# Performance work log

Measured on AMD Instinct MI355X. Metric: run time of the kernel, lower is better.

Reference implementation:

```python
import jax, jax.numpy as jnp
import numpy as np

B, C, H, W = 2, 128, 64, 64


def setup_inputs() -> dict:
    key = jax.random.key(0)
    ks = jax.random.split(key, 16)
    s = 1.0 / np.sqrt(C)
    d = {
        "x": jax.random.normal(ks[0], (B, C, H, W), jnp.float32),
        "y": jax.random.normal(ks[1], (B, C, H, W), jnp.float32),
    }
    names = ["qr", "qi", "kr", "ki", "vr", "vi"]
    for i, n in enumerate(names):
        d["W" + n] = jax.random.normal(ks[2 + 2 * i], (C, C), jnp.float32) * s
        d["b" + n] = jax.random.normal(ks[3 + 2 * i], (C,), jnp.float32) * s
    return d


def _lin(t, Wt, bt):
    # t: [b, n, c]; torch Linear: t @ W^T + b
    return jnp.einsum("bnc,dc->bnd", t, Wt) + bt


def reference(x, y, Wqr, bqr, Wqi, bqi, Wkr, bkr, Wki, bki, Wvr, bvr, Wvi, bvi):
    b, c, h, w = x.shape
    xf = jnp.fft.fft2(x)  # over last two axes (h, w)
    yf = jnp.fft.fft2(y)
    # b c h w -> b (h w) c
    def flat(t):
        return t.transpose(0, 2, 3, 1).reshape(b, h * w, c)
    xr, xi = flat(xf.real), flat(xf.imag)
    yr, yi = flat(yf.real), flat(yf.imag)

    Qr = _lin(xr, Wqr, bqr) - _lin(xi, Wqi, bqi)
    Qi = _lin(xi, Wqr, bqr) + _lin(xr, Wqi, bqi)
    Kr = _lin(yr, Wkr, bkr) - _lin(yi, Wki, bki)
    Ki = _lin(yi, Wkr, bkr) + _lin(yr, Wki, bki)
    Vr = _lin(yr, Wvr, bvr) - _lin(yi, Wvi, bvi)
    Vi = _lin(yi, Wvr, bvr) + _lin(yr, Wvi, bvi)

    sr = jnp.einsum("bnc,bmc->bnm", Qr, Kr) - jnp.einsum("bnc,bmc->bnm", Qi, Ki)
    si = jnp.einsum("bnc,bmc->bnm", Qr, Ki) + jnp.einsum("bnc,bmc->bnm", Qi, Kr)
    scores = jnp.sqrt(sr * sr + si * si + 1e-8)
    attn = jax.nn.softmax(scores, axis=-1)

    out_r = jnp.einsum("bnm,bmc->bnc", attn, Vr)
    out_i = jnp.einsum("bnm,bmc->bnc", attn, Vi)
    out_c = jax.lax.complex(out_r, out_i)
    # b (h w) c -> b c h w
    out_c = out_c.reshape(b, h, w, c).transpose(0, 3, 1, 2)
    return jnp.fft.ifft2(out_c).real
```

## Files before the change

kernel.cpp:

```cpp
#include <hip/hip_runtime.h>
#include <math.h>


#define PI2 6.283185307179586f

typedef __attribute__((ext_vector_type(8))) short short8;
typedef __attribute__((ext_vector_type(4))) float f32x4;

#define MFMA16(A,B,C) __builtin_amdgcn_mfma_f32_16x16x32_bf16((A),(B),(C),0,0,0)

__device__ inline unsigned short f2bf(float x){
  union{float f; unsigned int u;} a; a.f = x;
  unsigned int r = (a.u + 0x7fffu + ((a.u>>16)&1u)) >> 16;
  return (unsigned short)r;
}
__device__ inline float bf2f(unsigned short h){
  union{unsigned int u; float f;} a; a.u = ((unsigned int)h)<<16; return a.f;
}
__device__ inline short8 neg8(short8 x){
  union{short8 v; unsigned int u[4];} a; a.v = x;
  a.u[0]^=0x80008000u; a.u[1]^=0x80008000u; a.u[2]^=0x80008000u; a.u[3]^=0x80008000u;
  return a.v;
}
__device__ inline void gload_lds16(const void* g, void* lds){
  __builtin_amdgcn_global_load_lds((const __attribute__((address_space(1))) unsigned int*)g,
                                   (__attribute__((address_space(3))) unsigned int*)lds,
                                   16, 0, 0);
}

__global__ __launch_bounds__(256) void dft2_fwd_kernel(
    const float* __restrict__ x, const float* __restrict__ y,
    float* __restrict__ xr, float* __restrict__ xi,
    float* __restrict__ yr, float* __restrict__ yi)
{
  __shared__ float Xs[4096];
  __shared__ float Tr[4096], Ti[4096];
  __shared__ float twc[64], tws[64];
  int blk = blockIdx.x;
  const float* src; float *outr, *outi;
  int plane;
  if (blk < 256) { src = x; outr = xr; outi = xi; plane = blk; }
  else           { src = y; outr = yr; outi = yi; plane = blk - 256; }
  int b = plane >> 7, c = plane & 127;
  int t = threadIdx.x;
  if (t < 64) {
    float ang = -PI2 * (float)t / 64.0f;
    twc[t] = cosf(ang); tws[t] = sinf(ang);
  }
  const float* p = src + ((size_t)plane << 12);
  for (int i = t; i < 4096; i += 256) Xs[i] = p[i];
  __syncthreads();
  for (int j = 0; j < 16; j++) {
    int o = t + 256 * j; int h = o >> 6, wp = o & 63;
    float ar = 0.f, ai = 0.f;
    for (int w = 0; w < 64; w++) {
      int k = (w * wp) & 63;
      float v = Xs[h * 64 + w];
      ar = fmaf(v, twc[k], ar);
      ai = fmaf(v, tws[k], ai);
    }
    Tr[h * 64 + wp] = ar; Ti[h * 64 + wp] = ai;
  }
  __syncthreads();
  size_t ob = ((size_t)b * 4096) * 128 + c;
  for (int j = 0; j < 16; j++) {
    int o = t + 256 * j; int hp = o >> 6, wp = o & 63;
    float ar = 0.f, ai = 0.f;
    for (int h = 0; h < 64; h++) {
      int k = (h * hp) & 63;
      float cr = twc[k], ci = tws[k];
      float tr = Tr[h * 64 + wp], ti = Ti[h * 64 + wp];
      ar += tr * cr - ti * ci;
      ai += tr * ci + ti * cr;
    }
    int n = (hp << 6) + wp;
    outr[ob + (size_t)n * 128] = ar;
    outi[ob + (size_t)n * 128] = ai;
  }
}

__global__ __launch_bounds__(256) void proj_kernel(
    const float* __restrict__ xr, const float* __restrict__ xi,
    const float* __restrict__ yr, const float* __restrict__ yi,
    const float* __restrict__ Wqr, const float* __restrict__ bqr,
    const float* __restrict__ Wqi, const float* __restrict__ bqi,
    const float* __restrict__ Wkr, const float* __restrict__ bkr,
    const float* __restrict__ Wki, const float* __restrict__ bki,
    const float* __restrict__ Wvr, const float* __restrict__ bvr,
    const float* __restrict__ Wvi, const float* __restrict__ bvi,
    unsigned short* __restrict__ FQ, unsigned short* __restrict__ FK,
    unsigned short* __restrict__ FV)
{
  __shared__ float Asr[64 * 33], Asi[64 * 33], Wsr[128 * 33], Wsi[128 * 33];
  int nt = blockIdx.x, lin = blockIdx.y, b = blockIdx.z;
  const float *ar, *ai, *Wr, *Wi, *br_, *bi_;
  unsigned short* F;
  if (lin == 0)      { ar = xr; ai = xi; Wr = Wqr; Wi = Wqi; br_ = bqr; bi_ = bqi; F = FQ; }
  else if (lin == 1) { ar = yr; ai = yi; Wr = Wkr; Wi = Wki; br_ = bkr; bi_ = bki; F = FK; }
  else               { ar = yr; ai = yi; Wr = Wvr; Wi = Wvi; br_ = bvr; bi_ = bvi; F = FV; }
  int t = threadIdx.x; int td = t & 15, tn = t >> 4;
  int n0 = nt * 64;
  size_t abase = (size_t)b * 4096 * 128 + (size_t)n0 * 128;
  const size_t PS = (size_t)2 * 4096 * 128;
  float accr[4][8] = {}, acci[4][8] = {};
  for (int kk = 0; kk < 4; kk++) {
    __syncthreads();
    for (int idx = t; idx < 64 * 32; idx += 256) {
      int r = idx >> 5, ccol = idx & 31;
      Asr[r * 33 + ccol] = ar[abase + (size_t)r * 128 + kk * 32 + ccol];
      Asi[r * 33 + ccol] = ai[abase + (size_t)r * 128 + kk * 32 + ccol];
    }
    for (int idx = t; idx < 128 * 32; idx += 256) {
      int r = idx >> 5, ccol = idx & 31;
      Wsr[r * 33 + ccol] = Wr[(size_t)r * 128 + kk * 32 + ccol];
      Wsi[r * 33 + ccol] = Wi[(size_t)r * 128 + kk * 32 + ccol];
    }
    __syncthreads();
    for (int k = 0; k < 32; k++) {
      float a_r[4], a_i[4], w_r[8], w_i[8];
      #pragma unroll
      for (int i = 0; i < 4; i++) {
        a_r[i] = Asr[(tn * 4 + i) * 33 + k];
        a_i[i] = Asi[(tn * 4 + i) * 33 + k];
      }
      #pragma unroll
      for (int jj = 0; jj < 8; jj++) {
        w_r[jj] = Wsr[(td + 16 * jj) * 33 + k];
        w_i[jj] = Wsi[(td + 16 * jj) * 33 + k];
      }
      #pragma unroll
      for (int i = 0; i < 4; i++)
        #pragma unroll
        for (int jj = 0; jj < 8; jj++) {
          accr[i][jj] += a_r[i] * w_r[jj] - a_i[i] * w_i[jj];
          acci[i][jj] += a_i[i] * w_r[jj] + a_r[i] * w_i[jj];
        }
    }
  }
  for (int jj = 0; jj < 8; jj++) {
    int d = td + 16 * jj;
    float brd = br_[d], bid = bi_[d];
    #pragma unroll
    for (int i = 0; i < 4; i++) {
      int n = n0 + tn * 4 + i;
      float cr = accr[i][jj] + (brd - bid);
      float ci = acci[i][jj] + (brd + bid);
      size_t base = ((size_t)b * 4096 + n) * 128 + d;
      if (lin <= 1) {
        unsigned short rh = f2bf(cr); unsigned short rl = f2bf(cr - bf2f(rh));
        unsigned short ih = f2bf(ci); unsigned short il = f2bf(ci - bf2f(ih));
        F[0 * PS + base] = rh;
        F[1 * PS + base] = rl;
        F[2 * PS + base] = ih;
        F[3 * PS + base] = il;
      } else {
        F[0 * PS + base] = f2bf(cr);
        F[1 * PS + base] = f2bf(ci);
      }
    }
  }
}

__global__ __launch_bounds__(256) void kpack_kernel(
    const unsigned short* __restrict__ F, unsigned short* __restrict__ Kpk)
{
  int blk = blockIdx.x;
  int b = blk >> 6, mt = blk & 63;
  int t = threadIdx.x;
  size_t obase = (size_t)blk * 4096;
  #pragma unroll
  for (int k = 0; k < 16; k++) {
    int idx = t + 256 * k;
    int l = idx & 63, s = (idx >> 6) & 3, tml = (idx >> 8) & 3, a = idx >> 10;
    int n = mt * 64 + tml * 16 + (l & 15);
    int c0 = 32 * s + 8 * (l >> 4);
    const short8 v = *(const short8*)(F + (((size_t)(a * 2 + b) * 4096 + n) * 128 + c0));
    *(short8*)(Kpk + (obase + idx) * 8) = v;
  }
}

__global__ __launch_bounds__(256) void vpack32_kernel(
    const unsigned short* __restrict__ F, unsigned short* __restrict__ Vpk)
{
  __shared__ unsigned short Vs[2][128][128];
  int blk = blockIdx.x;
  int b = blk >> 5, mtp = blk & 31;
  int t = threadIdx.x;
  const size_t PS = (size_t)2 * 4096 * 128;
  #pragma unroll
  for (int k = 0; k < 16; k++) {
    int idx = t + 256 * k;
    int c8 = idx & 15, row = (idx >> 4) & 127, p = idx >> 11;
    short8 v = *(const short8*)(F + (size_t)p * PS +
                ((size_t)(b * 4096) + mtp * 128 + row) * 128 + c8 * 8);
    *(short8*)(&Vs[p][row][c8 * 8]) = v;
  }
  __syncthreads();
  size_t obase = (size_t)blk * 4096;
  #pragma unroll
  for (int k = 0; k < 16; k++) {
    int idx = t + 256 * k;
    int l2 = idx & 63, tc = (idx >> 6) & 15, w2 = idx >> 10;
    int g2 = l2 >> 4, c2 = l2 & 15;
    int cc = tc * 16 + c2; int p = cc >> 7; int cv = cc & 127;
    int rbase = (g2 >> 1) * 64 + 16 * w2 + 8 * (g2 & 1);
    short8 v;
    #pragma unroll
    for (int j = 0; j < 8; j++) v[j] = (short)Vs[p][rbase + j][cv];
    *(short8*)(Vpk + (obase + idx) * 8) = v;
  }
}

__global__ __launch_bounds__(256, 2) void attn_mfma_kernel(
    const unsigned short* __restrict__ FQ, const unsigned short* __restrict__ Kpk,
    const unsigned short* __restrict__ Vpk,
    float* __restrict__ Or_, float* __restrict__ Oi_)
{
  __shared__ __align__(16) short Klds[4][8192];
  __shared__ __align__(16) unsigned short Ppriv[4][16 * 40];
  __shared__ float Msh[4][16];
  __shared__ float Lsh[4][16];

  const int bi = blockIdx.x;
  const int xg = bi & 7;
  const int b = xg >> 2;
  const int qt2 = (bi >> 3) * 4 + (xg & 3);
  const int t = threadIdx.x;
  const int w = t >> 6, l = t & 63;
  const int g = l >> 4, c = l & 15;

  const size_t PS = (size_t)2 * 4096 * 128;
  short8 Qf[4][4];
  #pragma unroll
  for (int a = 0; a < 4; a++)
    #pragma unroll
    for (int s = 0; s < 4; s++)
      Qf[a][s] = *(const short8*)(FQ + (size_t)a * PS +
                 ((size_t)(b * 4096) + qt2 * 16 + c) * 128 + 32 * s + 8 * g);

  f32x4 O[16], Oe;
  #pragma unroll
  for (int tc = 0; tc < 16; tc++) O[tc] = (f32x4){0.f, 0.f, 0.f, 0.f};
  Oe = (f32x4){0.f, 0.f, 0.f, 0.f};
  float Mq = -3e38f;
  const short b1 = (short)0x3F80;
  const short8 ones = {b1, b1, b1, b1, b1, b1, b1, b1};
  const short8* Vp8 = (const short8*)Vpk;

  const char* KpkB = (const char*)Kpk;
  char* chunkB = (char*)&Klds[w][0];
  const short8* chunk8 = (const short8*)&Klds[w][0];

  auto STAGE = [&](int tile) {
    const char* src = KpkB + ((size_t)(b * 64 + tile) << 16);
    #pragma unroll
    for (int a = 0; a < 4; a++)
      #pragma unroll
      for (int s = 0; s < 4; s++)
        gload_lds16(src + (((a * 4 + w) * 4 + s) << 10) + l * 16,
                    chunkB + ((a * 4 + s) << 10));
  };

  STAGE(0);
  asm volatile("s_waitcnt vmcnt(0)" ::: "memory");
  __builtin_amdgcn_sched_barrier(0);

  f32x4 sE, sO;
  for (int mt = 0; mt < 64; mt++) {
    f32x4 sr = (f32x4){0, 0, 0, 0}, si = (f32x4){0, 0, 0, 0};
    #pragma unroll
    for (int s = 0; s < 4; s++) {
      short8 Arh = chunk8[(0 * 4 + s) * 64 + l];
      short8 Arl = chunk8[(1 * 4 + s) * 64 + l];
      short8 Aih = chunk8[(2 * 4 + s) * 64 + l];
      short8 Ail = chunk8[(3 * 4 + s) * 64 + l];
      short8 nqh = neg8(Qf[2][s]);
      short8 nql = neg8(Qf[3][s]);
      sr = MFMA16(Arh, Qf[0][s], sr);
      si = MFMA16(Arh, Qf[2][s], si);
      sr = MFMA16(Arh, Qf[1][s], sr);
      si = MFMA16(Arh, Qf[3][s], si);
      sr = MFMA16(Arl, Qf[0][s], sr);
      si = MFMA16(Arl, Qf[2][s], si);
      sr = MFMA16(Aih, nqh, sr);
      si = MFMA16(Aih, Qf[0][s], si);
      sr = MFMA16(Aih, nql, sr);
      si = MFMA16(Aih, Qf[1][s], si);
      sr = MFMA16(Ail, nqh, sr);
      si = MFMA16(Ail, Qf[0][s], si);
    }
    f32x4 s0;
    #pragma unroll
    for (int r = 0; r < 4; r++)
      s0[r] = sqrtf(sr[r] * sr[r] + si[r] * si[r] + 1e-8f);
    asm volatile("s_waitcnt lgkmcnt(0)" ::: "memory");
    __builtin_amdgcn_sched_barrier(0);
    if (mt + 1 < 64) STAGE(mt + 1);
    if ((mt & 1) == 0) {
      sE = s0;
    } else {
      sO = s0;
      float mloc = fmaxf(fmaxf(fmaxf(sE[0], sE[1]), fmaxf(sE[2], sE[3])),
                         fmaxf(fmaxf(sO[0], sO[1]), fmaxf(sO[2], sO[3])));
      mloc = fmaxf(mloc, __shfl_xor(mloc, 16));
      mloc = fmaxf(mloc, __shfl_xor(mloc, 32));
      float Mnew = fmaxf(Mq, mloc);
      float esc = __expf(Mq - Mnew);
      Mq = Mnew;
      f32x4 PE, PO;
      #pragma unroll
      for (int r = 0; r < 4; r++) {
        PE[r] = __expf(sE[r] - Mnew);
        PO[r] = __expf(sO[r] - Mnew);
      }
      unsigned int* pw0 = (unsigned int*)&Ppriv[w][c * 40 + 4 * g];
      pw0[0] = (unsigned int)f2bf(PE[0]) | ((unsigned int)f2bf(PE[1]) << 16);
      pw0[1] = (unsigned int)f2bf(PE[2]) | ((unsigned int)f2bf(PE[3]) << 16);
      unsigned int* pw1 = (unsigned int*)&Ppriv[w][c * 40 + 16 + 4 * g];
      pw1[0] = (unsigned int)f2bf(PO[0]) | ((unsigned int)f2bf(PO[1]) << 16);
      pw1[1] = (unsigned int)f2bf(PO[2]) | ((unsigned int)f2bf(PO[3]) << 16);
      f32x4 esc4;
      #pragma unroll
      for (int r = 0; r < 4; r++) esc4[r] = __shfl(esc, 4 * g + r);
      #pragma unroll
      for (int tc = 0; tc < 16; tc++)
        #pragma unroll
        for (int r = 0; r < 4; r++) O[tc][r] *= esc4[r];
      #pragma unroll
      for (int r = 0; r < 4; r++) Oe[r] *= esc4[r];
      short8 PA = *(const short8*)&Ppriv[w][c * 40 + 8 * g];
      const int mtp = mt >> 1;
      const size_t vb = ((size_t)(((b * 32 + mtp) * 4 + w) * 16)) * 64 + l;
      #pragma unroll
      for (int tc = 0; tc < 16; tc++) {
        short8 VB = Vp8[vb + (size_t)tc * 64];
        O[tc] = MFMA16(PA, VB, O[tc]);
      }
      Oe = MFMA16(PA, ones, Oe);
    }
    asm volatile("s_waitcnt vmcnt(0)" ::: "memory");
    __builtin_amdgcn_sched_barrier(0);
  }

  if (l < 16) Msh[w][l] = Mq;
  __syncthreads();
  float escw[4];
  #pragma unroll
  for (int r = 0; r < 4; r++) {
    int q = 4 * g + r;
    float mstar = fmaxf(fmaxf(Msh[0][q], Msh[1][q]), fmaxf(Msh[2][q], Msh[3][q]));
    escw[r] = __expf(Msh[w][q] - mstar);
  }
  if (c == 0) {
    #pragma unroll
    for (int r = 0; r < 4; r++) Lsh[w][4 * g + r] = Oe[r] * escw[r];
  }
  float* Oacc = (float*)&Klds[0][0];
  for (int round = 0; round < 4; round++) {
    if (w == round) {
      #pragma unroll
      for (int tc = 0; tc < 16; tc++)
        #pragma unroll
        for (int r = 0; r < 4; r++) {
          int idx = (4 * g + r) * 256 + tc * 16 + c;
          float v = O[tc][r] * escw[r];
          if (round == 0) Oacc[idx] = v; else Oacc[idx] += v;
        }
    }
    __syncthreads();
  }
  const size_t base = (size_t)b * 4096 * 128;
  const int col = w * 64 + l;
  #pragma unroll
  for (int q = 0; q < 16; q++) {
    float Lq = Lsh[0][q] + Lsh[1][q] + Lsh[2][q] + Lsh[3][q];
    float v = Oacc[q * 256 + col] / Lq;
    int row = qt2 * 16 + q;
    if (col < 128) Or_[base + (size_t)row * 128 + col] = v;
    else           Oi_[base + (size_t)row * 128 + col - 128] = v;
  }
}

__global__ __launch_bounds__(256) void idft2_kernel(
    const float* __restrict__ Or_, const float* __restrict__ Oi_,
    float* __restrict__ out)
{
  __shared__ float Ar[4096], Ai[4096], Tr[4096], Ti[4096];
  __shared__ float twc[64], tws[64];
  int plane = blockIdx.x; int b = plane >> 7, c = plane & 127;
  int t = threadIdx.x;
  if (t < 64) {
    float ang = PI2 * (float)t / 64.0f;
    twc[t] = cosf(ang); tws[t] = sinf(ang);
  }
  size_t ibase = (size_t)b * 4096 * 128 + c;
  for (int i = t; i < 4096; i += 256) {
    Ar[i] = Or_[ibase + (size_t)i * 128];
    Ai[i] = Oi_[ibase + (size_t)i * 128];
  }
  __syncthreads();
  for (int j = 0; j < 16; j++) {
    int o = t + 256 * j; int hp = o >> 6, w = o & 63;
    float tr = 0.f, ti = 0.f;
    for (int wp = 0; wp < 64; wp++) {
      int k = (wp * w) & 63;
      float cr = twc[k], ci = tws[k];
      float ar = Ar[hp * 64 + wp], ai = Ai[hp * 64 + wp];
      tr += ar * cr - ai * ci;
      ti += ai * cr + ar * ci;
    }
    Tr[hp * 64 + w] = tr; Ti[hp * 64 + w] = ti;
  }
  __syncthreads();
  size_t obase = ((size_t)plane) << 12;
  for (int j = 0; j < 16; j++) {
    int o = t + 256 * j; int h = o >> 6, w = o & 63;
    float acc = 0.f;
    for (int hp = 0; hp < 64; hp++) {
      int k = (hp * h) & 63;
      acc += Tr[hp * 64 + w] * twc[k] - Ti[hp * 64 + w] * tws[k];
    }
    out[obase + o] = acc * (1.0f / 4096.0f);
  }
}

extern "C" void kernel_launch(void* const* d_in, const int* in_sizes, int n_in,
                              void* d_out, int out_size, void* d_ws, size_t ws_size,
                              hipStream_t stream) {
  const float* x   = (const float*)d_in[0];
  const float* y   = (const float*)d_in[1];
  const float* Wqr = (const float*)d_in[2];  const float* bqr = (const float*)d_in[3];
  const float* Wqi = (const float*)d_in[4];  const float* bqi = (const float*)d_in[5];
  const float* Wkr = (const float*)d_in[6];  const float* bkr = (const float*)d_in[7];
  const float* Wki = (const float*)d_in[8];  const float* bki = (const float*)d_in[9];
  const float* Wvr = (const float*)d_in[10]; const float* bvr = (const float*)d_in[11];
  const float* Wvi = (const float*)d_in[12]; const float* bvi = (const float*)d_in[13];
  char* wsb = (char*)d_ws;
  if (ws_size < ((size_t)40 << 20)) return;
  unsigned short* FQ  = (unsigned short*)(wsb);
  unsigned short* FK  = (unsigned short*)(wsb + ((size_t)8  << 20));
  unsigned short* FV  = (unsigned short*)(wsb + ((size_t)16 << 20));
  float* xr = (float*)(wsb + ((size_t)20 << 20));
  float* xi = (float*)(wsb + ((size_t)24 << 20));
  float* yr = (float*)(wsb + ((size_t)28 << 20));
  float* yi = (float*)(wsb + ((size_t)32 << 20));
  unsigned short* Kpk = (unsigned short*)(wsb + ((size_t)28 << 20));
  unsigned short* Vpk = (unsigned short*)(wsb + ((size_t)36 << 20));
  float* Or_ = (float*)(wsb + ((size_t)20 << 20));
  float* Oi_ = (float*)(wsb + ((size_t)24 << 20));
  float* out = (float*)d_out;

  hipLaunchKernelGGL(dft2_fwd_kernel, dim3(512), dim3(256), 0, stream,
                     x, y, xr, xi, yr, yi);
  hipLaunchKernelGGL(proj_kernel, dim3(64, 3, 2), dim3(256), 0, stream,
                     xr, xi, yr, yi,
                     Wqr, bqr, Wqi, bqi, Wkr, bkr, Wki, bki, Wvr, bvr, Wvi, bvi,
                     FQ, FK, FV);
  hipLaunchKernelGGL(kpack_kernel, dim3(128), dim3(256), 0, stream, FK, Kpk);
  hipLaunchKernelGGL(vpack32_kernel, dim3(64), dim3(256), 0, stream, FV, Vpk);
  hipLaunchKernelGGL(attn_mfma_kernel, dim3(512), dim3(256), 0, stream,
                     FQ, Kpk, Vpk, Or_, Oi_);
  hipLaunchKernelGGL(idft2_kernel, dim3(256), dim3(256), 0, stream,
                     Or_, Oi_, out);
}
```

Measured before the change: 418.6 us.

## Software-pipeline attention loop, split PV across iterations, lazy softmax rescale

Restructures the attention main loop to process key tiles in pairs. Half of each PV MFMA batch is deferred into the next iteration so it overlaps the following QK computation and K staging. Rescaling of the output accumulators is skipped unless the running max grows by more than 8, since exp(s - M) stays bounded when M is stale. The Q negations are hoisted out of the loop, and the manual bf16 rounding is replaced with the v_cvt_pk_bf16_f32 instruction. This adds register pressure and relies on the stale-max bound holding numerically.

Result: no change. 424.7 us (+1.5%).

```diff
diff --git a/kernel.cpp b/kernel.cpp
--- a/kernel.cpp
+++ b/kernel.cpp
@@ -26,6 +26,11 @@
   __builtin_amdgcn_global_load_lds((const __attribute__((address_space(1))) unsigned int*)g,
                                    (__attribute__((address_space(3))) unsigned int*)lds,
                                    16, 0, 0);
+}
+__device__ inline unsigned int cvtpk_bf16(float lo, float hi){
+  unsigned int r;
+  asm("v_cvt_pk_bf16_f32 %0, %1, %2" : "=v"(r) : "v"(lo), "v"(hi));
+  return r;
 }
 
 __global__ __launch_bounds__(256) void dft2_fwd_kernel(
@@ -237,6 +242,9 @@
     for (int s = 0; s < 4; s++)
       Qf[a][s] = *(const short8*)(FQ + (size_t)a * PS +
                  ((size_t)(b * 4096) + qt2 * 16 + c) * 128 + 32 * s + 8 * g);
+  short8 nQ2[4], nQ3[4];
+  #pragma unroll
+  for (int s = 0; s < 4; s++) { nQ2[s] = neg8(Qf[2][s]); nQ3[s] = neg8(Qf[3][s]); }
 
   f32x4 O[16], Oe;
   #pragma unroll
@@ -260,13 +268,7 @@
         gload_lds16(src + (((a * 4 + w) * 4 + s) << 10) + l * 16,
                     chunkB + ((a * 4 + s) << 10));
   };
-
-  STAGE(0);
-  asm volatile("s_waitcnt vmcnt(0)" ::: "memory");
-  __builtin_amdgcn_sched_barrier(0);
-
-  f32x4 sE, sO;
-  for (int mt = 0; mt < 64; mt++) {
+  auto QK = [&](f32x4& sout) {
     f32x4 sr = (f32x4){0, 0, 0, 0}, si = (f32x4){0, 0, 0, 0};
     #pragma unroll
     for (int s = 0; s < 4; s++) {
@@ -274,73 +276,88 @@
       short8 Arl = chunk8[(1 * 4 + s) * 64 + l];
       short8 Aih = chunk8[(2 * 4 + s) * 64 + l];
       short8 Ail = chunk8[(3 * 4 + s) * 64 + l];
-      short8 nqh = neg8(Qf[2][s]);
-      short8 nql = neg8(Qf[3][s]);
       sr = MFMA16(Arh, Qf[0][s], sr);
       si = MFMA16(Arh, Qf[2][s], si);
       sr = MFMA16(Arh, Qf[1][s], sr);
       si = MFMA16(Arh, Qf[3][s], si);
       sr = MFMA16(Arl, Qf[0][s], sr);
       si = MFMA16(Arl, Qf[2][s], si);
-      sr = MFMA16(Aih, nqh, sr);
+      sr = MFMA16(Aih, nQ2[s], sr);
       si = MFMA16(Aih, Qf[0][s], si);
-      sr = MFMA16(Aih, nql, sr);
+      sr = MFMA16(Aih, nQ3[s], sr);
       si = MFMA16(Aih, Qf[1][s], si);
-      sr = MFMA16(Ail, nqh, sr);
+      sr = MFMA16(Ail, nQ2[s], sr);
       si = MFMA16(Ail, Qf[0][s], si);
     }
-    f32x4 s0;
     #pragma unroll
     for (int r = 0; r < 4; r++)
-      s0[r] = sqrtf(sr[r] * sr[r] + si[r] * si[r] + 1e-8f);
+      sout[r] = sqrtf(sr[r] * sr[r] + si[r] * si[r] + 1e-8f);
+  };
+  auto PVhalf = [&](int mtp, int h0) {
+    short8 PA = *(const short8*)&Ppriv[w][c * 40 + 8 * g];
+    const size_t vb = ((size_t)(((b * 32 + mtp) * 4 + w) * 16)) * 64 + l;
+    #pragma unroll
+    for (int tc = 0; tc < 8; tc++) {
+      short8 VB = Vp8[vb + (size_t)(h0 + tc) * 64];
+      O[h0 + tc] = MFMA16(PA, VB, O[h0 + tc]);
+    }
+    if (h0 == 8) Oe = MFMA16(PA, ones, Oe);
+  };
+
+  STAGE(0);
+  asm volatile("s_waitcnt vmcnt(0)" ::: "memory");
+  __builtin_amdgcn_sched_barrier(0);
+
+  f32x4 sE, sO;
+  for (int mtp = 0; mtp < 32; mtp++) {
+    QK(sE);
     asm volatile("s_waitcnt lgkmcnt(0)" ::: "memory");
     __builtin_amdgcn_sched_barrier(0);
-    if (mt + 1 < 64) STAGE(mt + 1);
-    if ((mt & 1) == 0) {
-      sE = s0;
-    } else {
-      sO = s0;
+    STAGE(2 * mtp + 1);
+    if (mtp > 0) PVhalf(mtp - 1, 8);
+    asm volatile("s_waitcnt vmcnt(0)" ::: "memory");
+    __builtin_amdgcn_sched_barrier(0);
+    QK(sO);
+    asm volatile("s_waitcnt lgkmcnt(0)" ::: "memory");
+    __builtin_amdgcn_sched_barrier(0);
+    if (mtp + 1 < 32) STAGE(2 * mtp + 2);
+    {
       float mloc = fmaxf(fmaxf(fmaxf(sE[0], sE[1]), fmaxf(sE[2], sE[3])),
                          fmaxf(fmaxf(sO[0], sO[1]), fmaxf(sO[2], sO[3])));
       mloc = fmaxf(mloc, __shfl_xor(mloc, 16));
       mloc = fmaxf(mloc, __shfl_xor(mloc, 32));
-      float Mnew = fmaxf(Mq, mloc);
-      float esc = __expf(Mq - Mnew);
-      Mq = Mnew;
+      if (!__all((int)(mloc <= Mq + 8.0f))) {
+        float Mnew = fmaxf(Mq, mloc);
+        float esc = __expf(Mq - Mnew);
+        Mq = Mnew;
+        f32x4 esc4;
+        #pragma unroll
+        for (int r = 0; r < 4; r++) esc4[r] = __shfl(esc, 4 * g + r);
+        #pragma unroll
+        for (int tc = 0; tc < 16; tc++)
+          #pragma unroll
+          for (int r = 0; r < 4; r++) O[tc][r] *= esc4[r];
+        #pragma unroll
+        for (int r = 0; r < 4; r++) Oe[r] *= esc4[r];
+      }
       f32x4 PE, PO;
       #pragma unroll
       for (int r = 0; r < 4; r++) {
-        PE[r] = __expf(sE[r] - Mnew);
-        PO[r] = __expf(sO[r] - Mnew);
+        PE[r] = __expf(sE[r] - Mq);
+        PO[r] = __expf(sO[r] - Mq);
       }
       unsigned int* pw0 = (unsigned int*)&Ppriv[w][c * 40 + 4 * g];
-      pw0[0] = (unsigned int)f2bf(PE[0]) | ((unsigned int)f2bf(PE[1]) << 16);
-      pw0[1] = (unsigned int)f2bf(PE[2]) | ((unsigned int)f2bf(PE[3]) << 16);
+      pw0[0] = cvtpk_bf16(PE[0], PE[1]);
+      pw0[1] = cvtpk_bf16(PE[2], PE[3]);
       unsigned int* pw1 = (unsigned int*)&Ppriv[w][c * 40 + 16 + 4 * g];
-      pw1[0] = (unsigned int)f2bf(PO[0]) | ((unsigned int)f2bf(PO[1]) << 16);
-      pw1[1] = (unsigned int)f2bf(PO[2]) | ((unsigned int)f2bf(PO[3]) << 16);
-      f32x4 esc4;
-      #pragma unroll
-      for (int r = 0; r < 4; r++) esc4[r] = __shfl(esc, 4 * g + r);
-      #pragma unroll
-      for (int tc = 0; tc < 16; tc++)
-        #pragma unroll
-        for (int r = 0; r < 4; r++) O[tc][r] *= esc4[r];
-      #pragma unroll
-      for (int r = 0; r < 4; r++) Oe[r] *= esc4[r];
-      short8 PA = *(const short8*)&Ppriv[w][c * 40 + 8 * g];
-      const int mtp = mt >> 1;
-      const size_t vb = ((size_t)(((b * 32 + mtp) * 4 + w) * 16)) * 64 + l;
-      #pragma unroll
-      for (int tc = 0; tc < 16; tc++) {
-        short8 VB = Vp8[vb + (size_t)tc * 64];
-        O[tc] = MFMA16(PA, VB, O[tc]);
-      }
-      Oe = MFMA16(PA, ones, Oe);
-    }
+      pw1[0] = cvtpk_bf16(PO[0], PO[1]);
+      pw1[1] = cvtpk_bf16(PO[2], PO[3]);
+    }
+    PVhalf(mtp, 0);
     asm volatile("s_waitcnt vmcnt(0)" ::: "memory");
     __builtin_amdgcn_sched_barrier(0);
   }
+  PVhalf(31, 8);
 
   if (l < 16) Msh[w][l] = Mq;
   __syncthreads();
```
